# Optimization experiments

Hardware: AMD Instinct MI355X
Metric: run time of the kernel (lower is better)

## Reference

```python
import jax, jax.numpy as jnp
import numpy as np

N = 50000        # nodes
E = 800000       # edges (before self-loops)
F_IN = 128       # input_features
HID = 160        # hidden_sf(5) * model_dim(32)
OUT_C = 128      # out_sf(4) * output_channels(32)
NGR = 64         # number of graphs in batch
OUT_DIM = 10
K = 5            # hops per SGConv


def setup_inputs() -> dict:
    key = jax.random.key(0)
    ks = jax.random.split(key, 12)
    x = jax.random.normal(ks[0], (N, F_IN), dtype=jnp.float32)
    edge_index = jax.random.randint(ks[1], (2, E), 0, N, dtype=jnp.int64)
    batch = jnp.sort(jax.random.randint(ks[2], (N,), 0, NGR, dtype=jnp.int64))
    s = 0.05
    W1 = jax.random.normal(ks[3], (F_IN, HID), dtype=jnp.float32) * s
    b1 = jnp.zeros((HID,), dtype=jnp.float32)
    W2 = jax.random.normal(ks[4], (HID, HID), dtype=jnp.float32) * s
    b2 = jnp.zeros((HID,), dtype=jnp.float32)
    W3 = jax.random.normal(ks[5], (HID, OUT_C), dtype=jnp.float32) * s
    b3 = jnp.zeros((OUT_C,), dtype=jnp.float32)
    fc_w = jax.random.normal(ks[6], (OUT_C, OUT_DIM), dtype=jnp.float32) * s
    fc_b = jnp.zeros((OUT_DIM,), dtype=jnp.float32)
    return {"x": x, "edge_index": edge_index, "batch": batch,
            "W1": W1, "b1": b1, "W2": W2, "b2": b2, "W3": W3, "b3": b3,
            "fc_w": fc_w, "fc_b": fc_b}


def reference(x, edge_index, batch, W1, b1, W2, b2, W3, b3, fc_w, fc_b):
    # gcn_norm: add self-loops, symmetric normalization D^-1/2 A D^-1/2
    loop = jnp.arange(N, dtype=edge_index.dtype)
    src = jnp.concatenate([edge_index[0], loop])   # [E+N]
    dst = jnp.concatenate([edge_index[1], loop])
    deg = jax.ops.segment_sum(jnp.ones(E + N, dtype=x.dtype), dst, num_segments=N)
    dinv = jnp.where(deg > 0, deg ** -0.5, 0.0)
    norm = (dinv[src] * dinv[dst])[:, None]        # [E+N, 1]

    def prop(h):
        # one hop of normalized propagation: gather at src, scatter-add at dst
        return jax.ops.segment_sum(h[src] * norm, dst, num_segments=N)

    def sgconv(h, W, b):
        for _ in range(K):
            h = prop(h)
        return h @ W + b

    h = sgconv(x, W1, b1)
    h = sgconv(h, W2, b2)
    h = sgconv(h, W3, b3)

    # global_mean_pool over batch indices
    counts = jax.ops.segment_sum(jnp.ones(N, dtype=h.dtype), batch, num_segments=NGR)
    pooled = jax.ops.segment_sum(h, batch, num_segments=NGR)
    pooled = pooled / jnp.maximum(counts, 1.0)[:, None]

    logits = pooled @ fc_w + fc_b
    return jax.nn.log_softmax(logits, axis=1)
```

## Files before the change

### kernel.cpp

```cpp
#include <hip/hip_runtime.h>

constexpr int N    = 50000;
constexpr int E    = 800000;
constexpr int NG   = 64;
constexpr int ODIM = 10;
constexpr int OUTC = 128;
constexpr int GP_BLOCKS = 256;
constexpr int SCAN_B = (N + 255) / 256;
constexpr int CS1B   = 784;
constexpr float SCALE    = 32768.0f;
constexpr float INVSCALE = 1.0f / SCALE;

typedef float floatx2 __attribute__((ext_vector_type(2)));

__device__ __forceinline__ void unp4(unsigned int u, float* f) {
    floatx2 lo = __builtin_amdgcn_cvt_pk_f32_fp8(u, false);
    floatx2 hi = __builtin_amdgcn_cvt_pk_f32_fp8(u, true);
    f[0] = lo.x; f[1] = lo.y; f[2] = hi.x; f[3] = hi.y;
}
__device__ __forceinline__ unsigned int pk4(float a, float b, float c, float d) {
    int r = __builtin_amdgcn_cvt_pk_fp8_f32(a, b, 0, false);
    r = __builtin_amdgcn_cvt_pk_fp8_f32(c, d, r, true);
    return (unsigned int)r;
}

__global__ void k_init_small(int* cntg, float* svec) {
    int i = threadIdx.x;
    if (i < NG) cntg[i] = 0;
    if (i < 128) svec[i] = 0.f;
}

__global__ void k_edge_count(const int* __restrict__ ei, int* degI8, int* cnt8,
                             int* __restrict__ pos_e) {
    int e = blockIdx.x * 256 + threadIdx.x;
    int q = blockIdx.x & 7;
    if (e < E) {
        int s = ei[e];
        int d = ei[E + e];
        atomicAdd(&degI8[q * N + d], 1);
        pos_e[e] = atomicAdd(&cnt8[q * N + s], 1);
    }
}

__global__ void k_scan1(const int* __restrict__ cnt8, int* __restrict__ base8,
                        int* __restrict__ off, int* bsum,
                        const int* __restrict__ degI8, float* wsq, float* sdeg) {
    __shared__ int buf[256];
    int tid = threadIdx.x;
    int i = blockIdx.x * 256 + tid;
    int total = 0;
    if (i < N) {
        int run = 0;
        #pragma unroll
        for (int q = 0; q < 8; ++q) {
            base8[q * N + i] = run;
            run += cnt8[q * N + i];
        }
        total = run;
        int deg = 1;
        #pragma unroll
        for (int q = 0; q < 8; ++q) deg += degI8[q * N + i];
        float d = (float)deg;
        wsq[i]  = 1.0f / d;
        sdeg[i] = sqrtf(d);
    }
    buf[tid] = total;
    __syncthreads();
    for (int s = 1; s < 256; s <<= 1) {
        int add = (tid >= s) ? buf[tid - s] : 0;
        __syncthreads();
        buf[tid] += add;
        __syncthreads();
    }
    if (i < N) off[i] = buf[tid] - total;
    if (tid == 255) bsum[blockIdx.x] = buf[255];
}

__global__ void k_scan2(int* bsum, int* off) {
    __shared__ int buf[256];
    int tid = threadIdx.x;
    int v = (tid < SCAN_B) ? bsum[tid] : 0;
    buf[tid] = v;
    __syncthreads();
    for (int s = 1; s < 256; s <<= 1) {
        int add = (tid >= s) ? buf[tid - s] : 0;
        __syncthreads();
        buf[tid] += add;
        __syncthreads();
    }
    if (tid < SCAN_B) bsum[tid] = buf[tid] - v;
    if (tid == 0) off[N] = E;
}

__global__ void k_scan3(int* off, const int* __restrict__ bsum) {
    int i = blockIdx.x * 256 + threadIdx.x;
    if (i < N) off[i] += bsum[blockIdx.x];
}

__global__ void k_cntg(const int* __restrict__ batch, int* cntg) {
    __shared__ int h[NG];
    if (threadIdx.x < NG) h[threadIdx.x] = 0;
    __syncthreads();
    int i = blockIdx.x * 256 + threadIdx.x;
    if (i < N) atomicAdd(&h[batch[i]], 1);
    __syncthreads();
    if (threadIdx.x < NG && h[threadIdx.x]) atomicAdd(&cntg[threadIdx.x], h[threadIdx.x]);
}

__global__ void k_fill(const int* __restrict__ ei, const int* __restrict__ off,
                       const int* __restrict__ base8, const int* __restrict__ pos_e,
                       int* __restrict__ mdst,
                       const int* __restrict__ batch, const int* __restrict__ cntg,
                       const float* __restrict__ sdeg, uint4* Z0) {
    int e = blockIdx.x * 256 + threadIdx.x;
    if (e < E) {
        int s = ei[e];
        int q = (e >> 8) & 7;
        mdst[off[s] + base8[q * N + s] + pos_e[e]] = ei[E + e];
    }
    if (e < N) {
        int i = e;
        int g = batch[i];
        int c = cntg[g]; if (c < 1) c = 1;
        float v = (SCALE / (float)c) / sdeg[i];
        unsigned int byte = (unsigned int)(__builtin_amdgcn_cvt_pk_fp8_f32(v, v, 0, false) & 0xFF);
        uint4 rows[4];
        #pragma unroll
        for (int q = 0; q < 4; ++q) rows[q] = make_uint4(0u, 0u, 0u, 0u);
        unsigned int* wp = (unsigned int*)rows;
        wp[g >> 2] = byte << (8 * (g & 3));
        #pragma unroll
        for (int q = 0; q < 4; ++q) Z0[(size_t)i * 4 + q] = rows[q];
    }
}

__device__ __forceinline__ void add16(float* acc, uint4 g) {
    float f[16];
    unp4(g.x, f); unp4(g.y, f + 4); unp4(g.z, f + 8); unp4(g.w, f + 12);
    #pragma unroll
    for (int k = 0; k < 16; ++k) acc[k] += f[k];
}

__global__ __launch_bounds__(256) void k_prop(
        const uint4* __restrict__ zin, uint2* __restrict__ zout,
        const int* __restrict__ off, const int* __restrict__ mdst,
        const float* __restrict__ wsq) {
    int t = blockIdx.x * 256 + threadIdx.x;
    int node = t >> 3;
    int sub  = (t >> 2) & 1;
    int c    = t & 3;
    if (node >= N) return;

    float acc[16];
    #pragma unroll
    for (int k = 0; k < 16; ++k) acc[k] = 0.f;

    int a = off[node], b = off[node + 1];
    int half = (b - a + 1) >> 1;
    int e  = sub ? a + half : a;
    int e1 = sub ? b : a + half;
    if (!sub) {
        add16(acc, zin[(size_t)node * 4 + c]);
    }
    for (; e + 7 < e1; e += 8) {
        int d0 = mdst[e],     d1 = mdst[e + 1], d2 = mdst[e + 2], d3 = mdst[e + 3];
        int d4 = mdst[e + 4], d5 = mdst[e + 5], d6 = mdst[e + 6], d7 = mdst[e + 7];
        uint4 g0 = zin[(size_t)d0 * 4 + c];
        uint4 g1 = zin[(size_t)d1 * 4 + c];
        uint4 g2 = zin[(size_t)d2 * 4 + c];
        uint4 g3 = zin[(size_t)d3 * 4 + c];
        uint4 g4 = zin[(size_t)d4 * 4 + c];
        uint4 g5 = zin[(size_t)d5 * 4 + c];
        uint4 g6 = zin[(size_t)d6 * 4 + c];
        uint4 g7 = zin[(size_t)d7 * 4 + c];
        add16(acc, g0); add16(acc, g1); add16(acc, g2); add16(acc, g3);
        add16(acc, g4); add16(acc, g5); add16(acc, g6); add16(acc, g7);
    }
    for (; e + 3 < e1; e += 4) {
        int d0 = mdst[e], d1 = mdst[e + 1], d2 = mdst[e + 2], d3 = mdst[e + 3];
        uint4 g0 = zin[(size_t)d0 * 4 + c];
        uint4 g1 = zin[(size_t)d1 * 4 + c];
        uint4 g2 = zin[(size_t)d2 * 4 + c];
        uint4 g3 = zin[(size_t)d3 * 4 + c];
        add16(acc, g0); add16(acc, g1); add16(acc, g2); add16(acc, g3);
    }
    for (; e < e1; ++e) {
        add16(acc, zin[(size_t)mdst[e] * 4 + c]);
    }

    #pragma unroll
    for (int k = 0; k < 16; ++k) acc[k] += __shfl_xor(acc[k], 4, 64);

    float ws = wsq[node];
    uint2 o;
    if (sub == 0) {
        o.x = pk4(ws * acc[0],  ws * acc[1],  ws * acc[2],  ws * acc[3]);
        o.y = pk4(ws * acc[4],  ws * acc[5],  ws * acc[6],  ws * acc[7]);
    } else {
        o.x = pk4(ws * acc[8],  ws * acc[9],  ws * acc[10], ws * acc[11]);
        o.y = pk4(ws * acc[12], ws * acc[13], ws * acc[14], ws * acc[15]);
    }
    zout[(size_t)node * 8 + c * 2 + sub] = o;
}

__global__ void k_colsum1(const unsigned int* __restrict__ Z,
                          const float* __restrict__ sdeg, float* __restrict__ part2) {
    __shared__ float red[256];
    int g = threadIdx.x & 63, sub = threadIdx.x >> 6;
    int w = g >> 2;
    int word = (g >> 1) & 1;
    int odd  = g & 1;
    float acc = 0.f;
    for (int i = blockIdx.x * 4 + sub; i < N; i += gridDim.x * 4) {
        unsigned int u = Z[(size_t)i * 16 + w];
        floatx2 p = word ? __builtin_amdgcn_cvt_pk_f32_fp8(u, true)
                         : __builtin_amdgcn_cvt_pk_f32_fp8(u, false);
        acc += (odd ? p.y : p.x) * sdeg[i];
    }
    red[threadIdx.x] = acc;
    __syncthreads();
    if (sub == 0)
        part2[g * CS1B + blockIdx.x] = red[g] + red[64 + g] + red[128 + g] + red[192 + g];
}

__global__ void k_colsum2(const float* __restrict__ part2, float* __restrict__ sdst) {
    __shared__ float red[256];
    int g = blockIdx.x, tid = threadIdx.x;
    float acc = 0.f;
    for (int b = tid; b < CS1B; b += 256) acc += part2[g * CS1B + b];
    red[tid] = acc;
    __syncthreads();
    for (int s = 128; s >= 1; s >>= 1) {
        if (tid < s) red[tid] += red[tid + s];
        __syncthreads();
    }
    if (tid == 0) sdst[g] = red[0] * INVSCALE;
}

__global__ __launch_bounds__(256) void k_gpart(
        const uint4* __restrict__ Z, const float4* __restrict__ X,
        const float* __restrict__ sdeg, float* part) {
    __shared__ unsigned int zr[32][16];
    __shared__ float xr[32][128];
    __shared__ float sd[32];
    int tid = threadIdx.x;
    int f4 = tid & 31;
    int gs = tid >> 5;
    float4 acc[8];
    #pragma unroll
    for (int k = 0; k < 8; ++k) acc[k] = make_float4(0.f, 0.f, 0.f, 0.f);

    int per = (N + gridDim.x - 1) / gridDim.x;
    int n0 = blockIdx.x * per;
    int n1 = n0 + per; if (n1 > N) n1 = N;

    for (int nb = n0; nb < n1; nb += 32) {
        __syncthreads();
        if (tid < 128) {
            int nn = tid >> 2, q = tid & 3;
            int node = nb + nn;
            uint4 zv = make_uint4(0u, 0u, 0u, 0u);
            if (node < n1) zv = Z[(size_t)node * 4 + q];
            ((uint4*)&zr[nn][0])[q] = zv;
        }
        if (tid >= 192 && tid < 224) {
            int node = nb + (tid - 192);
            sd[tid - 192] = (node < n1) ? sdeg[node] : 0.f;
        }
        #pragma unroll
        for (int r = 0; r < 4; ++r) {
            int l = r * 256 + tid;
            int nn = l >> 5, c4 = l & 31;
            int node = nb + nn;
            float4 xv = make_float4(0.f, 0.f, 0.f, 0.f);
            if (node < n1) xv = X[(size_t)node * 32 + c4];
            ((float4*)&xr[nn][0])[c4] = xv;
        }
        __syncthreads();
        for (int nn = 0; nn < 32; ++nn) {
            float sc = sd[nn];
            float4 xv = ((const float4*)&xr[nn][0])[f4];
            xv.x *= sc; xv.y *= sc; xv.z *= sc; xv.w *= sc;
            unsigned int za = zr[nn][gs * 2], zb = zr[nn][gs * 2 + 1];
            float zf[8];
            unp4(za, zf); unp4(zb, zf + 4);
            #pragma unroll
            for (int k = 0; k < 8; ++k) {
                acc[k].x += zf[k] * xv.x; acc[k].y += zf[k] * xv.y;
                acc[k].z += zf[k] * xv.z; acc[k].w += zf[k] * xv.w;
            }
        }
    }
    float4* dst = (float4*)(part + (size_t)blockIdx.x * 8192);
    #pragma unroll
    for (int k = 0; k < 8; ++k) dst[(gs * 8 + k) * 32 + f4] = acc[k];
}

__global__ void k_greduce(const float4* __restrict__ part, float4* G) {
    __shared__ float4 red[256];
    int tid = threadIdx.x;
    int o4 = blockIdx.x * 16 + (tid & 15);
    int slice = tid >> 4;
    float4 a = make_float4(0.f, 0.f, 0.f, 0.f);
    #pragma unroll 4
    for (int k = 0; k < GP_BLOCKS / 16; ++k) {
        float4 v = part[(size_t)(slice * (GP_BLOCKS / 16) + k) * 2048 + o4];
        a.x += v.x; a.y += v.y; a.z += v.z; a.w += v.w;
    }
    red[tid] = a;
    __syncthreads();
    for (int s = 128; s >= 16; s >>= 1) {
        if (tid < s) {
            float4 b = red[tid + s];
            red[tid].x += b.x; red[tid].y += b.y; red[tid].z += b.z; red[tid].w += b.w;
        }
        __syncthreads();
    }
    if (tid < 16) {
        float4 r = red[tid];
        G[o4] = make_float4(r.x * INVSCALE, r.y * INVSCALE, r.z * INVSCALE, r.w * INVSCALE);
    }
}

__global__ void k_pass1(const float* __restrict__ W1, const float* __restrict__ b1,
                        const float* __restrict__ W2, float* T1c) {
    int t = blockIdx.x * 256 + threadIdx.x;
    if (t >= 129 * 160) return;
    int m = t / 160, c = t - m * 160;
    const float* arow = (m < 128) ? (W1 + m * 160) : b1;
    float a = 0.f;
    for (int k = 0; k < 160; ++k) a += arow[k] * W2[k * 160 + c];
    T1c[t] = a;
}

__global__ void k_pass2(const float* __restrict__ T1c, const float* __restrict__ b2,
                        const float* __restrict__ W3, float* TWc) {
    int t = blockIdx.x * 256 + threadIdx.x;
    if (t >= 130 * 128) return;
    int m = t >> 7, c = t & 127;
    const float* arow = (m < 129) ? (T1c + m * 160) : b2;
    float a = 0.f;
    for (int k = 0; k < 160; ++k) a += arow[k] * W3[k * 128 + c];
    TWc[t] = a;
}

__global__ void k_pooled(const float* __restrict__ G, const float* __restrict__ TWc,
                         const float* __restrict__ b3, const float* __restrict__ svec,
                         float* pooled) {
    int t = blockIdx.x * 256 + threadIdx.x;
    if (t >= NG * OUTC) return;
    int g = t >> 7, f = t & 127;
    float a = b3[f] + svec[64 + g] * TWc[128 * 128 + f] + svec[g] * TWc[129 * 128 + f];
    for (int k = 0; k < 128; ++k) a += G[g * 128 + k] * TWc[k * 128 + f];
    pooled[t] = a;
}

__global__ void k_head(const float* __restrict__ pooled, const float* __restrict__ fcw,
                       const float* __restrict__ fcb, float* out) {
    __shared__ float lg[ODIM];
    int g = blockIdx.x, tid = threadIdx.x;
    if (tid < ODIM) {
        float a = fcb[tid];
        for (int k = 0; k < 128; ++k) a += pooled[g * 128 + k] * fcw[k * ODIM + tid];
        lg[tid] = a;
    }
    __syncthreads();
    if (tid == 0) {
        float mx = lg[0];
        for (int j = 1; j < ODIM; ++j) mx = fmaxf(mx, lg[j]);
        float sum = 0.f;
        for (int j = 0; j < ODIM; ++j) sum += expf(lg[j] - mx);
        float lse = mx + logf(sum);
        for (int j = 0; j < ODIM; ++j) out[g * ODIM + j] = lg[j] - lse;
    }
}

extern "C" void kernel_launch(void* const* d_in, const int* in_sizes, int n_in,
                              void* d_out, int out_size, void* d_ws, size_t ws_size,
                              hipStream_t stream) {
    const float* x    = (const float*)d_in[0];
    const int*   ei   = (const int*)d_in[1];
    const int*   batch= (const int*)d_in[2];
    const float* W1   = (const float*)d_in[3];
    const float* b1   = (const float*)d_in[4];
    const float* W2   = (const float*)d_in[5];
    const float* b2   = (const float*)d_in[6];
    const float* W3   = (const float*)d_in[7];
    const float* b3   = (const float*)d_in[8];
    const float* fcw  = (const float*)d_in[9];
    const float* fcb  = (const float*)d_in[10];
    float* out = (float*)d_out;

    char* p = (char*)d_ws;
    auto alloc = [&](size_t bytes) -> void* {
        void* r = (void*)p;
        p += (bytes + 255) & ~(size_t)255;
        return r;
    };
    int*   cnt8    = (int*)  alloc((size_t)8 * N * 4);
    int*   degI8   = (int*)  alloc((size_t)8 * N * 4);
    int*   base8   = (int*)  alloc((size_t)8 * N * 4);
    float* wsq     = (float*)alloc((size_t)N * 4);
    float* sdeg    = (float*)alloc((size_t)N * 4);
    int*   off     = (int*)  alloc((size_t)(N + 1) * 4);
    int*   bsum    = (int*)  alloc((size_t)SCAN_B * 4);
    int*   pos_e   = (int*)  alloc((size_t)E * 4);
    int*   mdst    = (int*)  alloc((size_t)E * 4);
    int*   cntg    = (int*)  alloc((size_t)NG * 4);
    float* svec    = (float*)alloc(128 * 4);
    unsigned char* Z0 = (unsigned char*)alloc((size_t)N * 64);
    unsigned char* Z1 = (unsigned char*)alloc((size_t)N * 64);
    float* part    = (float*)alloc((size_t)GP_BLOCKS * 8192 * 4);
    float* G       = (float*)alloc(8192 * 4);
    float* T1c     = (float*)alloc(129 * 160 * 4);
    float* TWc     = (float*)alloc(130 * 128 * 4);
    float* pooled  = (float*)alloc(64 * 128 * 4);

    int nb_n = (N + 255) / 256;
    int nb_e = (E + 255) / 256;
    (void)hipMemsetAsync(cnt8,  0, (size_t)8 * N * 4, stream);
    (void)hipMemsetAsync(degI8, 0, (size_t)8 * N * 4, stream);
    k_init_small<<<1, 256, 0, stream>>>(cntg, svec);
    k_edge_count<<<nb_e, 256, 0, stream>>>(ei, degI8, cnt8, pos_e);
    k_scan1<<<SCAN_B, 256, 0, stream>>>(cnt8, base8, off, bsum, degI8, wsq, sdeg);
    k_scan2<<<1, 256, 0, stream>>>(bsum, off);
    k_scan3<<<SCAN_B, 256, 0, stream>>>(off, bsum);
    k_cntg<<<nb_n, 256, 0, stream>>>(batch, cntg);
    k_fill<<<nb_e, 256, 0, stream>>>(ei, off, base8, pos_e, mdst, batch, cntg, sdeg, (uint4*)Z0);

    unsigned char* zc = Z0;
    unsigned char* zn = Z1;
    for (int hop = 1; hop <= 15; ++hop) {
        k_prop<<<(N * 8 + 255) / 256, 256, 0, stream>>>(
            (const uint4*)zc, (uint2*)zn, off, mdst, wsq);
        unsigned char* t = zc; zc = zn; zn = t;
        if (hop == 5) {
            k_colsum1<<<CS1B, 256, 0, stream>>>((const unsigned int*)zc, sdeg, part);
            k_colsum2<<<64, 256, 0, stream>>>(part, svec);
        }
        if (hop == 10) {
            k_colsum1<<<CS1B, 256, 0, stream>>>((const unsigned int*)zc, sdeg, part);
            k_colsum2<<<64, 256, 0, stream>>>(part, svec + 64);
        }
    }

    k_gpart<<<GP_BLOCKS, 256, 0, stream>>>((const uint4*)zc, (const float4*)x, sdeg, part);
    k_greduce<<<128, 256, 0, stream>>>((const float4*)part, (float4*)G);

    k_pass1<<<(129 * 160 + 255) / 256, 256, 0, stream>>>(W1, b1, W2, T1c);
    k_pass2<<<(130 * 128 + 255) / 256, 256, 0, stream>>>(T1c, b2, W3, TWc);
    k_pooled<<<32, 256, 0, stream>>>(G, TWc, b3, svec, pooled);
    k_head<<<NG, 64, 0, stream>>>(pooled, fcw, fcb, out);
}
```

Before: 506.7 us.

## Replace global-atomic edge counting with LDS-privatized range histograms

Edge degree and source counts move from global atomics on 8 replicated arrays into shared-memory histograms. Each block owns one edge chunk and one node range, so the two memsets go away and the per-block results are written directly. Every block reads its full chunk and skips indices outside its range, so the edge list is read 8 times in exchange for cheap LDS atomics. The scan now walks 16 chunks instead of 8, and the fill step derives the chunk from the edge index.

```diff
diff --git a/kernel.cpp b/kernel.cpp
--- a/kernel.cpp
+++ b/kernel.cpp
@@ -11,6 +11,13 @@
 constexpr float SCALE    = 32768.0f;
 constexpr float INVSCALE = 1.0f / SCALE;
 
+constexpr int CNT_C = 16;
+constexpr int CHUNK = E / CNT_C;
+constexpr int CNT_R = 8;
+constexpr int RANGE = N / CNT_R;
+constexpr int NV4   = CHUNK / 4;
+constexpr int HV4   = NV4 / 2;
+
 typedef float floatx2 __attribute__((ext_vector_type(2)));
 
 __device__ __forceinline__ void unp4(unsigned int u, float* f) {
@@ -30,21 +37,56 @@
     if (i < 128) svec[i] = 0.f;
 }
 
-__global__ void k_edge_count(const int* __restrict__ ei, int* degI8, int* cnt8,
-                             int* __restrict__ pos_e) {
-    int e = blockIdx.x * 256 + threadIdx.x;
-    int q = blockIdx.x & 7;
-    if (e < E) {
-        int s = ei[e];
-        int d = ei[E + e];
-        atomicAdd(&degI8[q * N + d], 1);
-        pos_e[e] = atomicAdd(&cnt8[q * N + s], 1);
-    }
-}
-
-__global__ void k_scan1(const int* __restrict__ cnt8, int* __restrict__ base8,
+__device__ __forceinline__ void cnt4_src(int4 v, int lo, int* h,
+                                         int* __restrict__ pos_e, int e) {
+    if ((unsigned)(v.x - lo) < (unsigned)RANGE) pos_e[e]     = atomicAdd(&h[v.x - lo], 1);
+    if ((unsigned)(v.y - lo) < (unsigned)RANGE) pos_e[e + 1] = atomicAdd(&h[v.y - lo], 1);
+    if ((unsigned)(v.z - lo) < (unsigned)RANGE) pos_e[e + 2] = atomicAdd(&h[v.z - lo], 1);
+    if ((unsigned)(v.w - lo) < (unsigned)RANGE) pos_e[e + 3] = atomicAdd(&h[v.w - lo], 1);
+}
+__device__ __forceinline__ void cnt4_dst(int4 v, int lo, int* h) {
+    if ((unsigned)(v.x - lo) < (unsigned)RANGE) atomicAdd(&h[v.x - lo], 1);
+    if ((unsigned)(v.y - lo) < (unsigned)RANGE) atomicAdd(&h[v.y - lo], 1);
+    if ((unsigned)(v.z - lo) < (unsigned)RANGE) atomicAdd(&h[v.z - lo], 1);
+    if ((unsigned)(v.w - lo) < (unsigned)RANGE) atomicAdd(&h[v.w - lo], 1);
+}
+
+__global__ __launch_bounds__(512) void k_count(const int* __restrict__ ei,
+        int* __restrict__ cnt16, int* __restrict__ deg16, int* __restrict__ pos_e) {
+    __shared__ int h[RANGE];
+    int bid  = blockIdx.x;
+    int c    = bid & 15;
+    int r    = (bid >> 4) & 7;
+    int kind = bid >> 7;
+    int tid  = threadIdx.x;
+    for (int i = tid; i < RANGE; i += 512) h[i] = 0;
+    __syncthreads();
+    int lo = r * RANGE;
+    const int4* src = (const int4*)(ei + (size_t)kind * E + (size_t)c * CHUNK);
+    int ebase = c * CHUNK;
+    if (kind == 0) {
+        for (int i = tid; i < HV4; i += 512) {
+            int4 a = src[i];
+            int4 b = src[i + HV4];
+            cnt4_src(a, lo, h, pos_e, ebase + i * 4);
+            cnt4_src(b, lo, h, pos_e, ebase + (i + HV4) * 4);
+        }
+    } else {
+        for (int i = tid; i < HV4; i += 512) {
+            int4 a = src[i];
+            int4 b = src[i + HV4];
+            cnt4_dst(a, lo, h);
+            cnt4_dst(b, lo, h);
+        }
+    }
+    __syncthreads();
+    int* dst = (kind == 0 ? cnt16 : deg16) + (size_t)c * N + lo;
+    for (int i = tid; i < RANGE; i += 512) dst[i] = h[i];
+}
+
+__global__ void k_scan1(const int* __restrict__ cnt16, int* __restrict__ base16,
                         int* __restrict__ off, int* bsum,
-                        const int* __restrict__ degI8, float* wsq, float* sdeg) {
+                        const int* __restrict__ deg16, float* wsq, float* sdeg) {
     __shared__ int buf[256];
     int tid = threadIdx.x;
     int i = blockIdx.x * 256 + tid;
@@ -52,14 +94,14 @@
     if (i < N) {
         int run = 0;
         #pragma unroll
-        for (int q = 0; q < 8; ++q) {
-            base8[q * N + i] = run;
-            run += cnt8[q * N + i];
+        for (int q = 0; q < CNT_C; ++q) {
+            base16[q * N + i] = run;
+            run += cnt16[q * N + i];
         }
         total = run;
         int deg = 1;
         #pragma unroll
-        for (int q = 0; q < 8; ++q) deg += degI8[q * N + i];
+        for (int q = 0; q < CNT_C; ++q) deg += deg16[q * N + i];
         float d = (float)deg;
         wsq[i]  = 1.0f / d;
         sdeg[i] = sqrtf(d);
@@ -108,15 +150,15 @@
 }
 
 __global__ void k_fill(const int* __restrict__ ei, const int* __restrict__ off,
-                       const int* __restrict__ base8, const int* __restrict__ pos_e,
+                       const int* __restrict__ base16, const int* __restrict__ pos_e,
                        int* __restrict__ mdst,
                        const int* __restrict__ batch, const int* __restrict__ cntg,
                        const float* __restrict__ sdeg, uint4* Z0) {
     int e = blockIdx.x * 256 + threadIdx.x;
     if (e < E) {
         int s = ei[e];
-        int q = (e >> 8) & 7;
-        mdst[off[s] + base8[q * N + s] + pos_e[e]] = ei[E + e];
+        int q = e / CHUNK;
+        mdst[off[s] + base16[q * N + s] + pos_e[e]] = ei[E + e];
     }
     if (e < N) {
         int i = e;
@@ -397,9 +439,9 @@
         p += (bytes + 255) & ~(size_t)255;
         return r;
     };
-    int*   cnt8    = (int*)  alloc((size_t)8 * N * 4);
-    int*   degI8   = (int*)  alloc((size_t)8 * N * 4);
-    int*   base8   = (int*)  alloc((size_t)8 * N * 4);
+    int*   cnt16   = (int*)  alloc((size_t)CNT_C * N * 4);
+    int*   deg16   = (int*)  alloc((size_t)CNT_C * N * 4);
+    int*   base16  = (int*)  alloc((size_t)CNT_C * N * 4);
     float* wsq     = (float*)alloc((size_t)N * 4);
     float* sdeg    = (float*)alloc((size_t)N * 4);
     int*   off     = (int*)  alloc((size_t)(N + 1) * 4);
@@ -418,15 +460,13 @@
 
     int nb_n = (N + 255) / 256;
     int nb_e = (E + 255) / 256;
-    (void)hipMemsetAsync(cnt8,  0, (size_t)8 * N * 4, stream);
-    (void)hipMemsetAsync(degI8, 0, (size_t)8 * N * 4, stream);
     k_init_small<<<1, 256, 0, stream>>>(cntg, svec);
-    k_edge_count<<<nb_e, 256, 0, stream>>>(ei, degI8, cnt8, pos_e);
-    k_scan1<<<SCAN_B, 256, 0, stream>>>(cnt8, base8, off, bsum, degI8, wsq, sdeg);
+    k_count<<<CNT_C * CNT_R * 2, 512, 0, stream>>>(ei, cnt16, deg16, pos_e);
+    k_scan1<<<SCAN_B, 256, 0, stream>>>(cnt16, base16, off, bsum, deg16, wsq, sdeg);
     k_scan2<<<1, 256, 0, stream>>>(bsum, off);
     k_scan3<<<SCAN_B, 256, 0, stream>>>(off, bsum);
     k_cntg<<<nb_n, 256, 0, stream>>>(batch, cntg);
-    k_fill<<<nb_e, 256, 0, stream>>>(ei, off, base8, pos_e, mdst, batch, cntg, sdeg, (uint4*)Z0);
+    k_fill<<<nb_e, 256, 0, stream>>>(ei, off, base16, pos_e, mdst, batch, cntg, sdeg, (uint4*)Z0);
 
     unsigned char* zc = Z0;
     unsigned char* zn = Z1;
```

Result: faster. 448.7 us (-11.5%).
